# Optimization experiments

Hardware: AMD Instinct MI355X
Metric: run time of the kernel (lower is better)

The kernel has to match this reference:

```python
import jax, jax.numpy as jnp
import numpy as np

N_NODES = 40000


def setup_inputs() -> dict:
    key = jax.random.key(0)
    k_h, k_w, k_b, k_s, k_d = jax.random.split(key, 5)
    in_feats, out_feats, n_edges = 128, 128, 640000
    h = jax.random.normal(k_h, (N_NODES, in_feats), dtype=jnp.float32)
    # nn.Linear(in_feats, out_feats): weight [out, in], bias [out]
    W = jax.random.normal(k_w, (out_feats, in_feats), dtype=jnp.float32) * (1.0 / np.sqrt(in_feats))
    b = jax.random.normal(k_b, (out_feats,), dtype=jnp.float32) * 0.01
    src = jax.random.randint(k_s, (n_edges,), 0, N_NODES, dtype=jnp.int32)
    dst = jax.random.randint(k_d, (n_edges,), 0, N_NODES, dtype=jnp.int32)
    return {"h": h, "W": W, "b": b, "src": src, "dst": dst}


def reference(h, W, b, src, dst):
    # update_all(copy_u('h','m'), sum('m','h_N')):
    # gather messages from source nodes, segment-sum into destination nodes.
    msgs = h[src]                                              # [E, in_feats] irregular gather
    agg = jax.ops.segment_sum(msgs, dst, num_segments=N_NODES)  # [N, in_feats] scatter-add
    # Source module applies the linear to h (agg is computed but unused there);
    # we return agg as a second output so the SpMM is observable.
    out = h @ W.T + b                                          # [N, out_feats]
    return out, agg
```

## Files before the change

kernel.cpp:

```cpp
#include <hip/hip_runtime.h>

#define FEAT   128
#define NQ     8
#define CAPR   16
#define SEGW   (NQ * CAPR)
#define RSMAX  640
#define NRANGE 64

typedef short bf16x8 __attribute__((ext_vector_type(8)));
typedef float f32x4  __attribute__((ext_vector_type(4)));

__device__ __forceinline__ unsigned pack_bf16x2(float x, float y) {
    unsigned ux = __float_as_uint(x);
    ux = (ux + 0x7fffu + ((ux >> 16) & 1u)) >> 16;
    unsigned uy = __float_as_uint(y);
    uy = (uy + 0x7fffu + ((uy >> 16) & 1u)) & 0xffff0000u;
    return uy | ux;
}

__device__ __forceinline__ bf16x8 pack8(float4 a, float4 b) {
    uint4 u = make_uint4(pack_bf16x2(a.x, a.y), pack_bf16x2(a.z, a.w),
                         pack_bf16x2(b.x, b.y), pack_bf16x2(b.z, b.w));
    return __builtin_bit_cast(bf16x8, u);
}

__device__ __forceinline__ f32x4 unpack2(unsigned x, unsigned y) {
    return (f32x4){__uint_as_float(x << 16), __uint_as_float(x & 0xffff0000u),
                   __uint_as_float(y << 16), __uint_as_float(y & 0xffff0000u)};
}

__global__ __launch_bounds__(512) void fused_kernel(
    const float* __restrict__ h, const float* __restrict__ W,
    const float* __restrict__ b, const int* __restrict__ src,
    const int* __restrict__ dst, float* __restrict__ out,
    uint4* __restrict__ hb4, unsigned short* __restrict__ bucket,
    unsigned char* __restrict__ counts,
    int nrows, int E, int RSv, int bin_blocks)
{
    __shared__ int            lcnt[RSMAX];
    __shared__ unsigned short lbkt[RSMAX * CAPR];

    const int bid = blockIdx.x;
    const int tid = threadIdx.x;

    if (bid < bin_blocks) {
        const int range = bid >> 3;
        const int rep   = bid & 7;
        const int base  = range * RSv;

        for (int i = tid; i < RSv; i += 512) lcnt[i] = 0;
        __syncthreads();

        const int EQ = (((E + NQ - 1) / NQ) + 3) & ~3;
        const int e0 = rep * EQ;
        int e1 = e0 + EQ; if (e1 > E) e1 = E;

        if (e0 < e1) {
            const int nq4 = (e1 - e0) >> 2;
            const int4* __restrict__ d4p = (const int4*)(dst + e0);
            const int4* __restrict__ s4p = (const int4*)(src + e0);
            int i = tid;
            for (; i + 512 * 3 < nq4; i += 512 * 4) {
                int4 dv[4], sv[4];
#pragma unroll
                for (int u = 0; u < 4; ++u) {
                    dv[u] = d4p[i + 512 * u];
                    sv[u] = s4p[i + 512 * u];
                }
#pragma unroll
                for (int u = 0; u < 4; ++u) {
                    int r, sl;
                    r = dv[u].x - base;
                    if ((unsigned)r < (unsigned)RSv) {
                        sl = atomicAdd(&lcnt[r], 1);
                        if (sl < CAPR) lbkt[r * CAPR + sl] = (unsigned short)sv[u].x;
                    }
                    r = dv[u].y - base;
                    if ((unsigned)r < (unsigned)RSv) {
                        sl = atomicAdd(&lcnt[r], 1);
                        if (sl < CAPR) lbkt[r * CAPR + sl] = (unsigned short)sv[u].y;
                    }
                    r = dv[u].z - base;
                    if ((unsigned)r < (unsigned)RSv) {
                        sl = atomicAdd(&lcnt[r], 1);
                        if (sl < CAPR) lbkt[r * CAPR + sl] = (unsigned short)sv[u].z;
                    }
                    r = dv[u].w - base;
                    if ((unsigned)r < (unsigned)RSv) {
                        sl = atomicAdd(&lcnt[r], 1);
                        if (sl < CAPR) lbkt[r * CAPR + sl] = (unsigned short)sv[u].w;
                    }
                }
            }
            for (; i < nq4; i += 512) {
                int4 dv = d4p[i], sv = s4p[i];
                int r, sl;
                r = dv.x - base;
                if ((unsigned)r < (unsigned)RSv) {
                    sl = atomicAdd(&lcnt[r], 1);
                    if (sl < CAPR) lbkt[r * CAPR + sl] = (unsigned short)sv.x;
                }
                r = dv.y - base;
                if ((unsigned)r < (unsigned)RSv) {
                    sl = atomicAdd(&lcnt[r], 1);
                    if (sl < CAPR) lbkt[r * CAPR + sl] = (unsigned short)sv.y;
                }
                r = dv.z - base;
                if ((unsigned)r < (unsigned)RSv) {
                    sl = atomicAdd(&lcnt[r], 1);
                    if (sl < CAPR) lbkt[r * CAPR + sl] = (unsigned short)sv.z;
                }
                r = dv.w - base;
                if ((unsigned)r < (unsigned)RSv) {
                    sl = atomicAdd(&lcnt[r], 1);
                    if (sl < CAPR) lbkt[r * CAPR + sl] = (unsigned short)sv.w;
                }
            }
            for (int e = e0 + (nq4 << 2) + tid; e < e1; e += 512) {
                int r = dst[e] - base;
                if ((unsigned)r < (unsigned)RSv) {
                    int sl = atomicAdd(&lcnt[r], 1);
                    if (sl < CAPR) lbkt[r * CAPR + sl] = (unsigned short)src[e];
                }
            }
        }
        __syncthreads();

        for (int i = tid; i < RSv; i += 512) {
            int c = lcnt[i]; if (c > CAPR) c = CAPR;
            counts[(size_t)(base + i) * NQ + rep] = (unsigned char)c;
        }
        const unsigned* l32 = (const unsigned*)lbkt;
        unsigned*       g32 = (unsigned*)bucket;
        for (int flat = tid; flat < RSv * (CAPR / 2); flat += 512) {
            int node = flat >> 3;
            int j    = flat & 7;
            g32[(size_t)(base + node) * (SEGW / 2) + rep * (CAPR / 2) + j] =
                l32[node * (CAPR / 2) + j];
        }
        return;
    }

    const int gbid = bid - bin_blocks;
    const int w    = tid >> 6;
    const int lane = tid & 63;
    const int m    = lane & 15, quad = lane >> 4;
    const int r0g  = gbid * 128 + (w >> 1) * 32;
    const int ch   = w & 1;
    if (r0g >= nrows) return;

    const float4* __restrict__ h4 = (const float4*)h;
    const float4* __restrict__ W4 = (const float4*)W;

    bf16x8 af[2][4];
#pragma unroll
    for (int mt = 0; mt < 2; ++mt) {
        int gr = r0g + mt * 16 + m;
#pragma unroll
        for (int ks = 0; ks < 4; ++ks) {
            float4 a0 = h4[(size_t)gr * 32 + ks * 8 + quad * 2];
            float4 a1 = h4[(size_t)gr * 32 + ks * 8 + quad * 2 + 1];
            af[mt][ks] = pack8(a0, a1);
        }
    }

    if (ch == 0) {
#pragma unroll
        for (int mt = 0; mt < 2; ++mt) {
            int gr = r0g + mt * 16 + m;
            if (gr < nrows) {
#pragma unroll
                for (int ks = 0; ks < 4; ++ks)
                    hb4[(size_t)gr * 16 + ks * 4 + quad] = __builtin_bit_cast(uint4, af[mt][ks]);
            }
        }
    }

    f32x4 acc[2][4];
#pragma unroll
    for (int mt = 0; mt < 2; ++mt)
#pragma unroll
        for (int nn = 0; nn < 4; ++nn) acc[mt][nn] = (f32x4){0.f, 0.f, 0.f, 0.f};

#pragma unroll
    for (int nn = 0; nn < 4; ++nn) {
        int c = (ch * 4 + nn) * 16 + m;
#pragma unroll
        for (int ks = 0; ks < 4; ++ks) {
            float4 b0 = W4[(size_t)c * 32 + ks * 8 + quad * 2];
            float4 b1 = W4[(size_t)c * 32 + ks * 8 + quad * 2 + 1];
            bf16x8 bf = pack8(b0, b1);
#pragma unroll
            for (int mt = 0; mt < 2; ++mt)
                acc[mt][nn] = __builtin_amdgcn_mfma_f32_16x16x32_bf16(
                    af[mt][ks], bf, acc[mt][nn], 0, 0, 0);
        }
    }

#pragma unroll
    for (int nn = 0; nn < 4; ++nn) {
        int col = (ch * 4 + nn) * 16 + m;
        float bias = b[col];
#pragma unroll
        for (int mt = 0; mt < 2; ++mt)
#pragma unroll
            for (int r = 0; r < 4; ++r) {
                int gr = r0g + mt * 16 + quad * 4 + r;
                if (gr < nrows)
                    __builtin_nontemporal_store(acc[mt][nn][r] + bias,
                                                &out[(size_t)gr * FEAT + col]);
            }
    }
}

__global__ __launch_bounds__(256) void gather_bucket_kernel(
    const uint4* __restrict__ hb4, const unsigned char* __restrict__ counts,
    const unsigned short* __restrict__ bucket, float* __restrict__ agg, int N)
{
    int gid  = blockIdx.x * 256 + threadIdx.x;
    int node = gid >> 6;
    int lane = gid & 63;
    if (node >= N) return;

    unsigned long long cw = *(const unsigned long long*)(counts + (size_t)node * NQ);
    int p1 = (int)(cw & 255);
    int p2 = p1 + (int)((cw >> 8) & 255);
    int p3 = p2 + (int)((cw >> 16) & 255);
    int p4 = p3 + (int)((cw >> 24) & 255);
    int p5 = p4 + (int)((cw >> 32) & 255);
    int p6 = p5 + (int)((cw >> 40) & 255);
    int p7 = p6 + (int)((cw >> 48) & 255);
    int deg = p7 + (int)((cw >> 56) & 255);
    if (deg > 64) deg = 64;

    int s = 0, ps = 0;
    if (lane >= p1) { s = 1; ps = p1; }
    if (lane >= p2) { s = 2; ps = p2; }
    if (lane >= p3) { s = 3; ps = p3; }
    if (lane >= p4) { s = 4; ps = p4; }
    if (lane >= p5) { s = 5; ps = p5; }
    if (lane >= p6) { s = 6; ps = p6; }
    if (lane >= p7) { s = 7; ps = p7; }

    int eid = 0;
    if (lane < deg)
        eid = bucket[(size_t)node * SEGW + s * CAPR + (lane - ps)];

    const int q = lane >> 4, ql = lane & 15;

    f32x4 al[4], ah[4];
#pragma unroll
    for (int k = 0; k < 4; ++k) { al[k] = (f32x4){0.f,0.f,0.f,0.f}; ah[k] = (f32x4){0.f,0.f,0.f,0.f}; }

    int t = 0;
    for (; t + 16 <= deg; t += 16) {
        int s0 = __shfl(eid, t + q);
        int s1 = __shfl(eid, t + 4 + q);
        int s2 = __shfl(eid, t + 8 + q);
        int s3 = __shfl(eid, t + 12 + q);
        uint4 v0 = hb4[(size_t)s0 * 16 + ql];
        uint4 v1 = hb4[(size_t)s1 * 16 + ql];
        uint4 v2 = hb4[(size_t)s2 * 16 + ql];
        uint4 v3 = hb4[(size_t)s3 * 16 + ql];
        al[0] += unpack2(v0.x, v0.y); ah[0] += unpack2(v0.z, v0.w);
        al[1] += unpack2(v1.x, v1.y); ah[1] += unpack2(v1.z, v1.w);
        al[2] += unpack2(v2.x, v2.y); ah[2] += unpack2(v2.z, v2.w);
        al[3] += unpack2(v3.x, v3.y); ah[3] += unpack2(v3.z, v3.w);
    }
    {
        int i0 = t + q, i1 = t + 4 + q, i2 = t + 8 + q, i3 = t + 12 + q;
        int s0 = __shfl(eid, i0 & 63);
        int s1 = __shfl(eid, i1 & 63);
        int s2 = __shfl(eid, i2 & 63);
        int s3 = __shfl(eid, i3 & 63);
        if (i0 < deg) { uint4 v = hb4[(size_t)s0 * 16 + ql]; al[0] += unpack2(v.x, v.y); ah[0] += unpack2(v.z, v.w); }
        if (i1 < deg) { uint4 v = hb4[(size_t)s1 * 16 + ql]; al[1] += unpack2(v.x, v.y); ah[1] += unpack2(v.z, v.w); }
        if (i2 < deg) { uint4 v = hb4[(size_t)s2 * 16 + ql]; al[2] += unpack2(v.x, v.y); ah[2] += unpack2(v.z, v.w); }
        if (i3 < deg) { uint4 v = hb4[(size_t)s3 * 16 + ql]; al[3] += unpack2(v.x, v.y); ah[3] += unpack2(v.z, v.w); }
    }
    al[0] += al[1]; ah[0] += ah[1];
    al[2] += al[3]; ah[2] += ah[3];
    al[0] += al[2]; ah[0] += ah[2];

#pragma unroll
    for (int j = 0; j < 4; ++j) {
        al[0][j] += __shfl_down(al[0][j], 32);
        ah[0][j] += __shfl_down(ah[0][j], 32);
        al[0][j] += __shfl_down(al[0][j], 16);
        ah[0][j] += __shfl_down(ah[0][j], 16);
    }

    if (q == 0) {
        f32x4* aggv = (f32x4*)agg;
        __builtin_nontemporal_store(al[0], &aggv[(size_t)node * 32 + ql * 2]);
        __builtin_nontemporal_store(ah[0], &aggv[(size_t)node * 32 + ql * 2 + 1]);
    }
}

__global__ __launch_bounds__(256, 2) void gemm_f32_kernel(
    const float* __restrict__ h, const float* __restrict__ W,
    const float* __restrict__ b, float* __restrict__ out, int nrows)
{
    __shared__ float4 wsh[128 * 8];
    __shared__ float4 hsh[64 * 8];
    const int tid = threadIdx.x;
    const int tx  = tid & 31;
    const int ty  = tid >> 5;
    const int r0  = blockIdx.x * 64;
    const float4* __restrict__ W4 = (const float4*)W;
    const float4* __restrict__ h4 = (const float4*)h;
    float acc[8][4];
#pragma unroll
    for (int i = 0; i < 8; ++i)
#pragma unroll
        for (int j = 0; j < 4; ++j) acc[i][j] = 0.f;
    for (int p = 0; p < 4; ++p) {
        if (p) __syncthreads();
#pragma unroll
        for (int l = 0; l < 4; ++l) {
            int flat = l * 256 + tid;
            int c = flat >> 3, kc = flat & 7;
            wsh[c * 8 + (kc ^ ((c >> 2) & 7))] = W4[c * 32 + p * 8 + kc];
        }
#pragma unroll
        for (int l = 0; l < 2; ++l) {
            int flat = l * 256 + tid;
            int r = flat >> 3, kc = flat & 7;
            int gr = r0 + r;
            float4 v = make_float4(0.f, 0.f, 0.f, 0.f);
            if (gr < nrows) v = h4[(size_t)gr * 32 + p * 8 + kc];
            hsh[r * 8 + (kc ^ ((r >> 2) & 7))] = v;
        }
        __syncthreads();
#pragma unroll
        for (int kc = 0; kc < 8; ++kc) {
            float4 wv[4], hv[8];
#pragma unroll
            for (int j = 0; j < 4; ++j) wv[j] = wsh[(4 * tx + j) * 8 + (kc ^ (tx & 7))];
#pragma unroll
            for (int i = 0; i < 8; ++i) {
                int r = 8 * ty + i;
                hv[i] = hsh[r * 8 + (kc ^ ((r >> 2) & 7))];
            }
#pragma unroll
            for (int i = 0; i < 8; ++i)
#pragma unroll
                for (int j = 0; j < 4; ++j) {
                    acc[i][j] += hv[i].x * wv[j].x;
                    acc[i][j] += hv[i].y * wv[j].y;
                    acc[i][j] += hv[i].z * wv[j].z;
                    acc[i][j] += hv[i].w * wv[j].w;
                }
        }
    }
    const float4 bj = ((const float4*)b)[tx];
    float4* out4 = (float4*)out;
#pragma unroll
    for (int i = 0; i < 8; ++i) {
        int gr = r0 + 8 * ty + i;
        if (gr < nrows) {
            float4 o;
            o.x = acc[i][0] + bj.x; o.y = acc[i][1] + bj.y;
            o.z = acc[i][2] + bj.z; o.w = acc[i][3] + bj.w;
            out4[(size_t)gr * 32 + tx] = o;
        }
    }
}

__global__ __launch_bounds__(256) void scatter_add_kernel(
    const float* __restrict__ h, const int* __restrict__ src,
    const int* __restrict__ dst, float* __restrict__ agg, int E)
{
    int gid  = blockIdx.x * 256 + threadIdx.x;
    int e    = gid >> 6;
    int lane = gid & 63;
    if (e >= E) return;
    int s = src[e];
    int d = dst[e];
    const float2* hp = (const float2*)(h + (size_t)s * FEAT);
    float2 v = hp[lane];
    float* ap = agg + (size_t)d * FEAT + 2 * lane;
    unsafeAtomicAdd(ap,     v.x);
    unsafeAtomicAdd(ap + 1, v.y);
}

extern "C" void kernel_launch(void* const* d_in, const int* in_sizes, int n_in,
                              void* d_out, int out_size, void* d_ws, size_t ws_size,
                              hipStream_t stream) {
    const float* h   = (const float*)d_in[0];
    const float* W   = (const float*)d_in[1];
    const float* b   = (const float*)d_in[2];
    const int*   src = (const int*)d_in[3];
    const int*   dst = (const int*)d_in[4];

    const int n = in_sizes[0] / FEAT;
    const int E = in_sizes[3];

    float* out = (float*)d_out;
    float* agg = out + (size_t)n * FEAT;

    size_t hb_bytes     = (size_t)n * FEAT * 2;
    size_t bucket_bytes = (size_t)n * SEGW * 2;
    size_t counts_bytes = (size_t)n * NQ;
    size_t need = hb_bytes + bucket_bytes + counts_bytes;

    bool fast = (ws_size >= need) && (n > 0) && ((n & 63) == 0) &&
                ((n >> 6) <= RSMAX) && (n <= 65536);

    if (fast) {
        uint4*          hb     = (uint4*)d_ws;
        unsigned short* bucket = (unsigned short*)((char*)d_ws + hb_bytes);
        unsigned char*  counts = (unsigned char*)((char*)d_ws + hb_bytes + bucket_bytes);

        int bin_blocks  = NRANGE * NQ;
        int gemm_blocks = (n + 127) / 128;
        fused_kernel<<<dim3(bin_blocks + gemm_blocks), dim3(512), 0, stream>>>(
            h, W, b, src, dst, out, hb, bucket, counts, n, E, n >> 6, bin_blocks);

        gather_bucket_kernel<<<dim3(n / 4), dim3(256), 0, stream>>>(
            hb, counts, bucket, agg, n);
    } else {
        gemm_f32_kernel<<<dim3((n + 63) / 64), dim3(256), 0, stream>>>(h, W, b, out, n);
        (void)hipMemsetAsync(agg, 0, (size_t)n * FEAT * sizeof(float), stream);
        int nblocks = (int)(((long long)E * 64 + 255) / 256);
        scatter_add_kernel<<<dim3(nblocks), dim3(256), 0, stream>>>(h, src, dst, agg, E);
    }
}
```

Baseline: 150.1 us.

## Halve binning ranges, compact per-lane edge atomics, and set occupancy hint

Binning blocks now cover twice as many destination rows each (32 ranges instead of 64), so each block scans the full edge list half as often in total, at the cost of twice the LDS bucket footprint. The four-way unrolled per-edge atomic insertion is replaced by a mask-driven loop that lets each lane work through only its in-range edges, so a wavefront spends fewer divergent passes on sparse hits. A launch-bounds minimum of four blocks per CU is added. The larger LDS use (about 45 KB per block) may limit how many bin blocks fit on a CU and may conflict with that occupancy hint.

```diff
diff --git a/kernel.cpp b/kernel.cpp
--- a/kernel.cpp
+++ b/kernel.cpp
@@ -4,8 +4,8 @@
 #define NQ     8
 #define CAPR   16
 #define SEGW   (NQ * CAPR)
-#define RSMAX  640
-#define NRANGE 64
+#define RSMAX  1280
+#define NRANGE 32
 
 typedef short bf16x8 __attribute__((ext_vector_type(8)));
 typedef float f32x4  __attribute__((ext_vector_type(4)));
@@ -29,7 +29,7 @@
                    __uint_as_float(y << 16), __uint_as_float(y & 0xffff0000u)};
 }
 
-__global__ __launch_bounds__(512) void fused_kernel(
+__global__ __launch_bounds__(512, 4) void fused_kernel(
     const float* __restrict__ h, const float* __restrict__ W,
     const float* __restrict__ b, const int* __restrict__ src,
     const int* __restrict__ dst, float* __restrict__ out,
@@ -69,51 +69,49 @@
                 }
 #pragma unroll
                 for (int u = 0; u < 4; ++u) {
-                    int r, sl;
-                    r = dv[u].x - base;
-                    if ((unsigned)r < (unsigned)RSv) {
-                        sl = atomicAdd(&lcnt[r], 1);
-                        if (sl < CAPR) lbkt[r * CAPR + sl] = (unsigned short)sv[u].x;
-                    }
-                    r = dv[u].y - base;
-                    if ((unsigned)r < (unsigned)RSv) {
-                        sl = atomicAdd(&lcnt[r], 1);
-                        if (sl < CAPR) lbkt[r * CAPR + sl] = (unsigned short)sv[u].y;
-                    }
-                    r = dv[u].z - base;
-                    if ((unsigned)r < (unsigned)RSv) {
-                        sl = atomicAdd(&lcnt[r], 1);
-                        if (sl < CAPR) lbkt[r * CAPR + sl] = (unsigned short)sv[u].z;
-                    }
-                    r = dv[u].w - base;
-                    if ((unsigned)r < (unsigned)RSv) {
-                        sl = atomicAdd(&lcnt[r], 1);
-                        if (sl < CAPR) lbkt[r * CAPR + sl] = (unsigned short)sv[u].w;
+                    int r0 = dv[u].x - base, r1 = dv[u].y - base;
+                    int r2 = dv[u].z - base, r3 = dv[u].w - base;
+                    unsigned m = ((unsigned)r0 < (unsigned)RSv ? 1u : 0u) |
+                                 ((unsigned)r1 < (unsigned)RSv ? 2u : 0u) |
+                                 ((unsigned)r2 < (unsigned)RSv ? 4u : 0u) |
+                                 ((unsigned)r3 < (unsigned)RSv ? 8u : 0u);
+                    while (__any(m != 0u)) {
+                        int k  = __ffs(m) - 1;
+                        int ra = (k & 1) ? r1 : r0;
+                        int rb = (k & 1) ? r3 : r2;
+                        int rr = (k & 2) ? rb : ra;
+                        int sa = (k & 1) ? sv[u].y : sv[u].x;
+                        int sb = (k & 1) ? sv[u].w : sv[u].z;
+                        int ss = (k & 2) ? sb : sa;
+                        if (m) {
+                            m &= m - 1u;
+                            int sl = atomicAdd(&lcnt[rr], 1);
+                            if (sl < CAPR) lbkt[rr * CAPR + sl] = (unsigned short)ss;
+                        }
                     }
                 }
             }
             for (; i < nq4; i += 512) {
                 int4 dv = d4p[i], sv = s4p[i];
-                int r, sl;
-                r = dv.x - base;
-                if ((unsigned)r < (unsigned)RSv) {
-                    sl = atomicAdd(&lcnt[r], 1);
-                    if (sl < CAPR) lbkt[r * CAPR + sl] = (unsigned short)sv.x;
-                }
-                r = dv.y - base;
-                if ((unsigned)r < (unsigned)RSv) {
-                    sl = atomicAdd(&lcnt[r], 1);
-                    if (sl < CAPR) lbkt[r * CAPR + sl] = (unsigned short)sv.y;
-                }
-                r = dv.z - base;
-                if ((unsigned)r < (unsigned)RSv) {
-                    sl = atomicAdd(&lcnt[r], 1);
-                    if (sl < CAPR) lbkt[r * CAPR + sl] = (unsigned short)sv.z;
-                }
-                r = dv.w - base;
-                if ((unsigned)r < (unsigned)RSv) {
-                    sl = atomicAdd(&lcnt[r], 1);
-                    if (sl < CAPR) lbkt[r * CAPR + sl] = (unsigned short)sv.w;
+                int r0 = dv.x - base, r1 = dv.y - base;
+                int r2 = dv.z - base, r3 = dv.w - base;
+                unsigned m = ((unsigned)r0 < (unsigned)RSv ? 1u : 0u) |
+                             ((unsigned)r1 < (unsigned)RSv ? 2u : 0u) |
+                             ((unsigned)r2 < (unsigned)RSv ? 4u : 0u) |
+                             ((unsigned)r3 < (unsigned)RSv ? 8u : 0u);
+                while (__any(m != 0u)) {
+                    int k  = __ffs(m) - 1;
+                    int ra = (k & 1) ? r1 : r0;
+                    int rb = (k & 1) ? r3 : r2;
+                    int rr = (k & 2) ? rb : ra;
+                    int sa = (k & 1) ? sv.y : sv.x;
+                    int sb = (k & 1) ? sv.w : sv.z;
+                    int ss = (k & 2) ? sb : sa;
+                    if (m) {
+                        m &= m - 1u;
+                        int sl = atomicAdd(&lcnt[rr], 1);
+                        if (sl < CAPR) lbkt[rr * CAPR + sl] = (unsigned short)ss;
+                    }
                 }
             }
             for (int e = e0 + (nq4 << 2) + tid; e < e1; e += 512) {
@@ -404,8 +402,8 @@
     size_t counts_bytes = (size_t)n * NQ;
     size_t need = hb_bytes + bucket_bytes + counts_bytes;
 
-    bool fast = (ws_size >= need) && (n > 0) && ((n & 63) == 0) &&
-                ((n >> 6) <= RSMAX) && (n <= 65536);
+    bool fast = (ws_size >= need) && (n > 0) && ((n & 31) == 0) &&
+                ((n >> 5) <= RSMAX) && (n <= 65536);
 
     if (fast) {
         uint4*          hb     = (uint4*)d_ws;
@@ -415,7 +413,7 @@
         int bin_blocks  = NRANGE * NQ;
         int gemm_blocks = (n + 127) / 128;
         fused_kernel<<<dim3(bin_blocks + gemm_blocks), dim3(512), 0, stream>>>(
-            h, W, b, src, dst, out, hb, bucket, counts, n, E, n >> 6, bin_blocks);
+            h, W, b, src, dst, out, hb, bucket, counts, n, E, n >> 5, bin_blocks);
 
         gather_bucket_kernel<<<dim3(n / 4), dim3(256), 0, stream>>>(
             hb, counts, bucket, agg, n);
```

New measurement: 154.4 us. +2.9%, slower.
